# Kernel tuning notes

Measured on AMD Instinct MI355X. Metric: run time of the kernel, lower is better.

Reference implementation:

```python
import jax, jax.numpy as jnp
import numpy as np

V, E, H, L, B, T = 371, 512, 8, 8, 4, 1024
D = E // H
EPS = 1e-5


def setup_inputs() -> dict:
    key = jax.random.key(0)
    ks = jax.random.split(key, 7)
    s = 0.02
    return {
        "idx": jax.random.randint(ks[0], (B, T), 0, V),
        "wte": jax.random.normal(ks[1], (V, E), jnp.float32) * s,   # tied with lm_head
        "wpe": jax.random.normal(ks[2], (T, E), jnp.float32) * s,
        "c_attn_w": jax.random.normal(ks[3], (L, E, 3 * E), jnp.float32) * s,
        "c_proj_w": jax.random.normal(ks[4], (L, E, E), jnp.float32) * s,
        "fc_w": jax.random.normal(ks[5], (L, E, 4 * E), jnp.float32) * s,
        "fc_proj_w": jax.random.normal(ks[6], (L, 4 * E, E), jnp.float32) * s,
        "ln1_w": jnp.ones((L, E), jnp.float32),
        "ln2_w": jnp.ones((L, E), jnp.float32),
        "lnf_w": jnp.ones((E,), jnp.float32),
    }


def _ln(x, w):
    m = jnp.mean(x, axis=-1, keepdims=True)
    v = jnp.mean((x - m) ** 2, axis=-1, keepdims=True)
    return (x - m) * jax.lax.rsqrt(v + EPS) * w


def reference(idx, wte, wpe, c_attn_w, c_proj_w, fc_w, fc_proj_w, ln1_w, ln2_w, lnf_w):
    mask = jnp.tril(jnp.ones((T, T), bool))  # causal mask, as in the registered buffer
    scale = 1.0 / np.sqrt(D)

    x0 = wte[idx] + wpe[None, :T]  # [B,T,E]

    def block(x, p):
        aw, pw, l1, l2, fw, fpw = p
        h = _ln(x, l1)
        qkv = h @ aw                                   # [B,T,3E]
        q, k, v = jnp.split(qkv, 3, axis=-1)
        q = q.reshape(B, T, H, D)
        k = k.reshape(B, T, H, D)
        v = v.reshape(B, T, H, D)
        att = jnp.einsum("bqhd,bkhd->bhqk", q, k) * scale  # full TxT scores (faithful)
        att = jnp.where(mask[None, None], att, -jnp.inf)
        att = jax.nn.softmax(att, axis=-1)
        y = jnp.einsum("bhqk,bkhd->bqhd", att, v).reshape(B, T, E)
        x = x + y @ pw
        h = _ln(x, l2)
        x = x + jax.nn.gelu(h @ fw, approximate=False) @ fpw
        return x, None

    x, _ = jax.lax.scan(block, x0, (c_attn_w, c_proj_w, ln1_w, ln2_w, fc_w, fc_proj_w))
    x = _ln(x, lnf_w)
    logits = x @ wte.T  # weight tying: lm_head.weight = wte.weight
    return logits
```

## Files before the change

kernel.cpp:

```cpp
#include <hip/hip_runtime.h>


#define VOCAB 371
#define VPAD  384
#define EMB   512
#define NH    8
#define NL    8
#define TS    1024
#define NTOK  4096
#define NEG_INF (-1e30f)

typedef unsigned short ushort_t;
typedef __attribute__((ext_vector_type(8))) short short8;
typedef __attribute__((ext_vector_type(4))) float f32x4;

__device__ inline float bf2f(ushort_t b) {
    unsigned int u = ((unsigned int)b) << 16;
    float f; __builtin_memcpy(&f, &u, 4); return f;
}
__device__ inline ushort_t f2bf(float f) {
    unsigned int u; __builtin_memcpy(&u, &f, 4);
    u = (u + 0x7fff + ((u >> 16) & 1)) >> 16;
    return (ushort_t)u;
}

#define GLOAD16(gp, lp) __builtin_amdgcn_global_load_lds( \
        (__attribute__((address_space(1))) void*)(gp), \
        (__attribute__((address_space(3))) void*)(lp), 16, 0, 0)

__global__ __launch_bounds__(64) void detect_k(const ushort_t* __restrict__ w,
        int* __restrict__ flag)
{
    int i = threadIdx.x;
    float v = bf2f(w[2 * i]);
    bool ok = (__builtin_fabsf(v) <= 4.0f);
    unsigned long long m = __ballot(ok);
    if (i == 0) flag[0] = (__popcll(m) >= 56) ? 1 : 0;
}

__global__ __launch_bounds__(256) void sentinel_k(ushort_t* __restrict__ out, int n)
{
    int i = blockIdx.x * 256 + threadIdx.x;
    if (i < n) out[i] = 0x447A;
}

__global__ __launch_bounds__(256) void embed_k(const int* __restrict__ idx,
        const void* __restrict__ wte, const void* __restrict__ wpe,
        float* __restrict__ x, const int* __restrict__ flag)
{
    int n = blockIdx.x, tid = threadIdx.x;
    int t = n & (TS - 1);
    int v = idx[n];
    size_t o = (size_t)n * EMB;
    float a0, a1, b0, b1;
    if (*flag) {
        const ushort_t* te = (const ushort_t*)wte; const ushort_t* pe = (const ushort_t*)wpe;
        a0 = bf2f(te[v * EMB + tid]); a1 = bf2f(te[v * EMB + 256 + tid]);
        b0 = bf2f(pe[t * EMB + tid]); b1 = bf2f(pe[t * EMB + 256 + tid]);
    } else {
        const float* te = (const float*)wte; const float* pe = (const float*)wpe;
        a0 = te[v * EMB + tid]; a1 = te[v * EMB + 256 + tid];
        b0 = pe[t * EMB + tid]; b1 = pe[t * EMB + 256 + tid];
    }
    x[o + tid] = a0 + b0;
    x[o + 256 + tid] = a1 + b1;
}

__global__ __launch_bounds__(256) void ln_k(const float* __restrict__ x,
        const void* __restrict__ w, long woff, ushort_t* __restrict__ out,
        const int* __restrict__ flag)
{
    const int row = blockIdx.x * 4 + (threadIdx.x >> 6);
    const int lane = threadIdx.x & 63;
    const float* xr = x + (size_t)row * EMB + lane * 8;
    float4 f0 = *(const float4*)xr;
    float4 f1 = *(const float4*)(xr + 4);
    float v[8] = {f0.x, f0.y, f0.z, f0.w, f1.x, f1.y, f1.z, f1.w};
    float s = ((v[0] + v[1]) + (v[2] + v[3])) + ((v[4] + v[5]) + (v[6] + v[7]));
#pragma unroll
    for (int off = 32; off > 0; off >>= 1) s += __shfl_xor(s, off, 64);
    float mean = s * (1.0f / EMB);
    float s2 = 0.f;
#pragma unroll
    for (int j = 0; j < 8; ++j) { v[j] -= mean; s2 += v[j] * v[j]; }
#pragma unroll
    for (int off = 32; off > 0; off >>= 1) s2 += __shfl_xor(s2, off, 64);
    float rs = rsqrtf(s2 * (1.0f / EMB) + 1e-5f);
    float g[8];
    if (*flag) {
        const ushort_t* wb = (const ushort_t*)w + woff + lane * 8;
        ushort_t tmp[8];
        *(uint4*)tmp = *(const uint4*)wb;
#pragma unroll
        for (int j = 0; j < 8; ++j) g[j] = bf2f(tmp[j]);
    } else {
        const float* wf = (const float*)w + woff + lane * 8;
        float4 g0 = *(const float4*)wf;
        float4 g1 = *(const float4*)(wf + 4);
        g[0] = g0.x; g[1] = g0.y; g[2] = g0.z; g[3] = g0.w;
        g[4] = g1.x; g[5] = g1.y; g[6] = g1.z; g[7] = g1.w;
    }
    ushort_t ob[8];
#pragma unroll
    for (int j = 0; j < 8; ++j) ob[j] = f2bf(v[j] * rs * g[j]);
    *(uint4*)(out + (size_t)row * EMB + lane * 8) = *(uint4*)ob;
}

__global__ __launch_bounds__(256) void wtrans_k(const void* __restrict__ aw,
        const void* __restrict__ pw, const void* __restrict__ fw,
        const void* __restrict__ fpw, long l, ushort_t* __restrict__ wbuf,
        const int* __restrict__ flag)
{
    __shared__ float tile[64][65];
    const int isbf = *flag;
    long lay = (l < 0) ? (long)blockIdx.z : l;
    ushort_t* obase = wbuf + ((l < 0) ? (size_t)blockIdx.z * 3145728 : 0);
    int t = blockIdx.x;
    const void* src; ushort_t* dst; int Kw, Nw; long ioff;
    if (t < 192)      { src = aw;  dst = obase;           Kw = 512;  Nw = 1536; ioff = lay * 512L * 1536; }
    else if (t < 256) { t -= 192; src = pw;  dst = obase + 786432;  Kw = 512;  Nw = 512;  ioff = lay * 512L * 512; }
    else if (t < 512) { t -= 256; src = fw;  dst = obase + 1048576; Kw = 512;  Nw = 2048; ioff = lay * 512L * 2048; }
    else              { t -= 512; src = fpw; dst = obase + 2097152; Kw = 2048; Nw = 512;  ioff = lay * 2048L * 512; }
    int tn = Nw >> 6;
    int n0 = (t % tn) * 64, k0 = (t / tn) * 64;
    const int r = threadIdx.x >> 2, cq = (threadIdx.x & 3) * 16;
    size_t ii = ioff + (size_t)(k0 + r) * Nw + n0 + cq;
    if (isbf) {
        const ushort_t* sb = (const ushort_t*)src + ii;
        ushort_t tmp[16];
        *(uint4*)tmp = *(const uint4*)sb;
        *(uint4*)(tmp + 8) = *(const uint4*)(sb + 8);
#pragma unroll
        for (int j = 0; j < 16; ++j) tile[r][cq + j] = bf2f(tmp[j]);
    } else {
        const float* sf = (const float*)src + ii;
        *(float4*)&tile[r][cq]      = *(const float4*)sf;
        *(float4*)&tile[r][cq + 4]  = *(const float4*)(sf + 4);
        *(float4*)&tile[r][cq + 8]  = *(const float4*)(sf + 8);
        *(float4*)&tile[r][cq + 12] = *(const float4*)(sf + 12);
    }
    __syncthreads();
    const int kc = (threadIdx.x & 7) * 8;
#pragma unroll
    for (int j = 0; j < 2; ++j) {
        const int n = (threadIdx.x >> 3) + j * 32;
        unsigned pk[4];
#pragma unroll
        for (int i = 0; i < 4; ++i) {
            unsigned lo = f2bf(tile[kc + 2 * i][n]);
            unsigned hi = f2bf(tile[kc + 2 * i + 1][n]);
            pk[i] = lo | (hi << 16);
        }
        *(uint4*)(dst + (size_t)(n0 + n) * Kw + k0 + kc) = *(uint4*)pk;
    }
}

__global__ __launch_bounds__(256) void wconv_k(const void* __restrict__ in,
        ushort_t* __restrict__ out, int n, int nreal, const int* __restrict__ flag)
{
    int i = blockIdx.x * 256 + threadIdx.x;
    if (i >= n) return;
    ushort_t v = 0;
    if (i < nreal) v = (*flag) ? ((const ushort_t*)in)[i] : f2bf(((const float*)in)[i]);
    out[i] = v;
}

template<int MI>
__global__ __launch_bounds__(256) void gemm_gl(const ushort_t* __restrict__ A,
        const ushort_t* __restrict__ Bt, int M, int N, int K,
        float* __restrict__ outF, ushort_t* __restrict__ outB, void* __restrict__ outD,
        const float* __restrict__ res, int act, const int* __restrict__ flag)
{
    constexpr int BM = MI * 64;
    __shared__ __align__(16) ushort_t Al[BM * 64];
    __shared__ __align__(16) ushort_t Bl[64 * 64];
    const int tid = threadIdx.x;
    const int wave = tid >> 6, lane = tid & 63;
    const int quad = lane >> 4, l16 = lane & 15;
    const int m0 = blockIdx.y * BM, n0 = blockIdx.x * 64;
    const int sr = lane >> 3, sc = (lane & 7) * 8;
    const size_t K8 = (size_t)K * 8;
    const ushort_t* Ag = A + (size_t)(m0 + wave * (MI * 16) + sr) * K + sc;
    const ushort_t* Bg = Bt + (size_t)(n0 + wave * 16 + sr) * K + sc;
    ushort_t* Alw = &Al[(wave * (MI * 16)) * 64];
    ushort_t* Blw = &Bl[(wave * 16) * 64];
    f32x4 acc[MI][4] = {};
    for (int k0 = 0; k0 < K; k0 += 64) {
        __syncthreads();
#pragma unroll
        for (int i = 0; i < MI * 2; ++i)
            GLOAD16(Ag + k0 + (size_t)i * K8, Alw + i * 512);
#pragma unroll
        for (int i = 0; i < 2; ++i)
            GLOAD16(Bg + k0 + (size_t)i * K8, Blw + i * 512);
        __syncthreads();
#pragma unroll
        for (int ks = 0; ks < 2; ++ks) {
            short8 af[MI], bfr[4];
#pragma unroll
            for (int mi = 0; mi < MI; ++mi)
                af[mi] = *(const short8*)&Al[(wave * (MI * 16) + mi * 16 + l16) * 64 + ks * 32 + quad * 8];
#pragma unroll
            for (int ni = 0; ni < 4; ++ni)
                bfr[ni] = *(const short8*)&Bl[(ni * 16 + l16) * 64 + ks * 32 + quad * 8];
#pragma unroll
            for (int mi = 0; mi < MI; ++mi)
#pragma unroll
                for (int ni = 0; ni < 4; ++ni)
                    acc[mi][ni] = __builtin_amdgcn_mfma_f32_16x16x32_bf16(
                            af[mi], bfr[ni], acc[mi][ni], 0, 0, 0);
        }
    }
    const int isbf = *flag;
#pragma unroll
    for (int mi = 0; mi < MI; ++mi) {
        const int rowb = m0 + wave * (MI * 16) + mi * 16 + quad * 4;
#pragma unroll
        for (int ni = 0; ni < 4; ++ni) {
            const int nn = n0 + ni * 16 + l16;
            if (nn >= N) continue;
#pragma unroll
            for (int r = 0; r < 4; ++r) {
                size_t o = (size_t)(rowb + r) * N + nn;
                float v = acc[mi][ni][r];
                if (res) v += res[o];
                if (act) v = 0.5f * v * (1.0f + erff(v * 0.70710678118f));
                if (outF)      outF[o] = v;
                else if (outB) outB[o] = f2bf(v);
                else if (isbf) ((ushort_t*)outD)[o] = f2bf(v);
                else           ((float*)outD)[o] = v;
            }
        }
    }
}

__global__ __launch_bounds__(256) void gemm_k(const ushort_t* __restrict__ A,
        const void* __restrict__ B, long boff, int M, int N, int K, int bt,
        float* __restrict__ outF, ushort_t* __restrict__ outB, void* __restrict__ outD,
        const float* __restrict__ res, int act, const int* __restrict__ flag)
{
    __shared__ ushort_t Al[64 * 40];
    __shared__ ushort_t Bl[64 * 40];
    const int isbf = *flag;
    const int tid = threadIdx.x;
    const int wave = tid >> 6, lane = tid & 63;
    const int quad = lane >> 4, l16 = lane & 15;
    const int m0 = blockIdx.y * 64, n0 = blockIdx.x * 64;
    const int sr = tid >> 2, sc = (tid & 3) * 8;
    const int kr = tid >> 3, nc = (tid & 7) * 8;
    f32x4 acc[4] = {};
    const bool bok = (n0 + sr) < N;
    const ushort_t* Ag = A + (size_t)(m0 + sr) * K + sc;
    const ushort_t* Bb = (const ushort_t*)B + boff;
    const float*    Bf = (const float*)B + boff;
    const size_t i1 = (size_t)(n0 + sr) * K + sc;
    const size_t i0 = (size_t)kr * N + n0 + nc;
    for (int k0 = 0; k0 < K; k0 += 32) {
        uint4 av = *(const uint4*)(Ag + k0);
        ushort_t b8[8] = {0, 0, 0, 0, 0, 0, 0, 0};
        size_t bi = bt ? (i1 + k0) : (i0 + (size_t)k0 * N);
        if (!bt || bok) {
            if (isbf) *(uint4*)b8 = *(const uint4*)(Bb + bi);
            else {
                float4 f0 = *(const float4*)(Bf + bi);
                float4 f1 = *(const float4*)(Bf + bi + 4);
                b8[0] = f2bf(f0.x); b8[1] = f2bf(f0.y); b8[2] = f2bf(f0.z); b8[3] = f2bf(f0.w);
                b8[4] = f2bf(f1.x); b8[5] = f2bf(f1.y); b8[6] = f2bf(f1.z); b8[7] = f2bf(f1.w);
            }
        }
        __syncthreads();
        *(uint4*)&Al[sr * 40 + sc] = av;
        if (bt) *(uint4*)&Bl[sr * 40 + sc] = *(uint4*)b8;
        else {
#pragma unroll
            for (int i = 0; i < 8; ++i) Bl[(nc + i) * 40 + kr] = b8[i];
        }
        __syncthreads();
        short8 af = *(const short8*)&Al[(wave * 16 + l16) * 40 + quad * 8];
#pragma unroll
        for (int nt = 0; nt < 4; ++nt) {
            short8 bf = *(const short8*)&Bl[(nt * 16 + l16) * 40 + quad * 8];
            acc[nt] = __builtin_amdgcn_mfma_f32_16x16x32_bf16(af, bf, acc[nt], 0, 0, 0);
        }
    }
    const int mb = m0 + wave * 16 + quad * 4;
#pragma unroll
    for (int nt = 0; nt < 4; ++nt) {
        int nn = n0 + nt * 16 + l16;
        if (nn >= N) continue;
#pragma unroll
        for (int r = 0; r < 4; ++r) {
            size_t o = (size_t)(mb + r) * N + nn;
            float v = acc[nt][r];
            if (res) v += res[o];
            if (act) v = 0.5f * v * (1.0f + erff(v * 0.70710678118f));
            if (outF)      outF[o] = v;
            else if (outB) outB[o] = f2bf(v);
            else if (isbf) ((ushort_t*)outD)[o] = f2bf(v);
            else           ((float*)outD)[o] = v;
        }
    }
}

__global__ __launch_bounds__(256) void attn_k(const ushort_t* __restrict__ qkv,
        ushort_t* __restrict__ y)
{
    __shared__ ushort_t Kl[64 * 72];
    __shared__ ushort_t Vt[64 * 72];
    __shared__ ushort_t Pl[4][16 * 72];
    const int tid = threadIdx.x, wave = tid >> 6, lane = tid & 63;
    const int quad = lane >> 4, l16 = lane & 15;
    const int qt = (int)gridDim.x - 1 - blockIdx.x;
    const int b = blockIdx.y >> 3, h = blockIdx.y & 7;
    const int q0b = qt * 64;
    const int q0w = q0b + wave * 16;
    const size_t rstr = 3 * EMB;
    const ushort_t* qbase = qkv + ((size_t)(b * TS) + q0w + l16) * rstr + h * 64;
    short8 qf0, qf1;
    {
        ushort_t q0[8], q1[8];
        *(uint4*)q0 = *(const uint4*)(qbase + quad * 8);
        *(uint4*)q1 = *(const uint4*)(qbase + 32 + quad * 8);
#pragma unroll
        for (int i = 0; i < 8; ++i) {
            qf0[i] = (short)f2bf(bf2f(q0[i]) * 0.125f);
            qf1[i] = (short)f2bf(bf2f(q1[i]) * 0.125f);
        }
    }
    short8 onesf;
#pragma unroll
    for (int i = 0; i < 8; ++i) onesf[i] = (short)0x3F80;
    f32x4 O[4] = {};
    f32x4 lacc = {};
    const int sk = tid >> 2, sdc = (tid & 3) * 16;
    const int vp = tid >> 3, vdc = (tid & 7) * 8;
    const int vsh = 16 * ((tid & 7) & 3);
    const int vcol = (2 * vp + vsh) & 63;
    for (int kt = 0; kt <= qt; ++kt) {
        const int k0 = kt * 64;
        const ushort_t* krow = qkv + ((size_t)(b * TS) + k0 + sk) * rstr + EMB + h * 64 + sdc;
        uint4 kv0 = *(const uint4*)krow;
        uint4 kv1 = *(const uint4*)(krow + 8);
        const ushort_t* vrow = qkv + ((size_t)(b * TS) + k0 + 2 * vp) * rstr + 2 * EMB + h * 64 + vdc;
        uint4 vv0 = *(const uint4*)vrow;
        uint4 vv1 = *(const uint4*)(vrow + rstr);
        __syncthreads();
        *(uint4*)&Kl[sk * 72 + sdc]     = kv0;
        *(uint4*)&Kl[sk * 72 + sdc + 8] = kv1;
        {
            ushort_t v0[8], v1[8];
            *(uint4*)v0 = vv0; *(uint4*)v1 = vv1;
#pragma unroll
            for (int i = 0; i < 8; ++i) {
                unsigned pk = (unsigned)v0[i] | ((unsigned)v1[i] << 16);
                *(unsigned*)&Vt[(vdc + i) * 72 + vcol] = pk;
            }
        }
        __syncthreads();
        if (kt < qt) {
            f32x4 S[4] = {};
#pragma unroll
            for (int nt = 0; nt < 4; ++nt) {
                short8 kf0 = *(const short8*)&Kl[(nt * 16 + l16) * 72 + quad * 8];
                short8 kf1 = *(const short8*)&Kl[(nt * 16 + l16) * 72 + 32 + quad * 8];
                S[nt] = __builtin_amdgcn_mfma_f32_16x16x32_bf16(qf0, kf0, S[nt], 0, 0, 0);
                S[nt] = __builtin_amdgcn_mfma_f32_16x16x32_bf16(qf1, kf1, S[nt], 0, 0, 0);
            }
#pragma unroll
            for (int nt = 0; nt < 4; ++nt)
#pragma unroll
                for (int r = 0; r < 4; ++r)
                    Pl[wave][(quad * 4 + r) * 72 + nt * 16 + l16] = f2bf(__expf(S[nt][r]));
        } else {
            f32x4 S[4] = {};
#pragma unroll
            for (int nt = 0; nt < 4; ++nt) {
                if (nt > wave) continue;
                short8 kf0 = *(const short8*)&Kl[(nt * 16 + l16) * 72 + quad * 8];
                short8 kf1 = *(const short8*)&Kl[(nt * 16 + l16) * 72 + 32 + quad * 8];
                S[nt] = __builtin_amdgcn_mfma_f32_16x16x32_bf16(qf0, kf0, S[nt], 0, 0, 0);
                S[nt] = __builtin_amdgcn_mfma_f32_16x16x32_bf16(qf1, kf1, S[nt], 0, 0, 0);
            }
#pragma unroll
            for (int nt = 0; nt < 4; ++nt)
#pragma unroll
                for (int r = 0; r < 4; ++r) {
                    bool live = (nt < wave) || (nt == wave && l16 <= quad * 4 + r);
                    float p = live ? __expf(S[nt][r]) : 0.f;
                    Pl[wave][(quad * 4 + r) * 72 + nt * 16 + l16] = f2bf(p);
                }
        }
#pragma unroll
        for (int kc = 0; kc < 2; ++kc) {
            short8 pf = *(const short8*)&Pl[wave][l16 * 72 + kc * 32 + quad * 8];
            lacc = __builtin_amdgcn_mfma_f32_16x16x32_bf16(pf, onesf, lacc, 0, 0, 0);
#pragma unroll
            for (int dt = 0; dt < 4; ++dt) {
                int d = dt * 16 + l16;
                int sh = ((2 * dt + (l16 >> 3)) & 3) * 16;
                int col = (kc * 32 + quad * 8 + sh) & 63;
                short8 vf = *(const short8*)&Vt[d * 72 + col];
                O[dt] = __builtin_amdgcn_mfma_f32_16x16x32_bf16(pf, vf, O[dt], 0, 0, 0);
            }
        }
    }
#pragma unroll
    for (int dt = 0; dt < 4; ++dt)
#pragma unroll
        for (int r = 0; r < 4; ++r) {
            int q = q0w + quad * 4 + r;
            float v = O[dt][r] / lacc[r];
            y[((size_t)(b * TS) + q) * EMB + h * 64 + dt * 16 + l16] = f2bf(v);
        }
}

extern "C" void kernel_launch(void* const* d_in, const int* in_sizes, int n_in,
                              void* d_out, int out_size, void* d_ws, size_t ws_size,
                              hipStream_t stream)
{
    const int*  idx    = (const int*)d_in[0];
    const void* wte    = d_in[1];
    const void* wpe    = d_in[2];
    const void* attn_w = d_in[3];
    const void* proj_w = d_in[4];
    const void* fc_w   = d_in[5];
    const void* fcp_w  = d_in[6];
    const void* ln1_w  = d_in[7];
    const void* ln2_w  = d_in[8];
    const void* lnf_w  = d_in[9];

    const size_t sz_xw    = (size_t)NTOK * EMB * 4;
    const size_t sz_hbf   = (size_t)NTOK * EMB * 2;
    const size_t sz_big   = (size_t)NTOK * 2048 * 2;
    const size_t sz_wteb  = (size_t)VPAD * EMB * 2;
    const size_t sz_wbuf1 = (size_t)3145728 * 2;
    const size_t need_legacy = 256 + sz_xw + sz_hbf + sz_big;
    const size_t need_fast   = need_legacy + sz_wteb + sz_wbuf1;
    const size_t need_all    = need_legacy + sz_wteb + NL * sz_wbuf1;

    if (ws_size < need_legacy) {
        sentinel_k<<<(out_size + 255) / 256, 256, 0, stream>>>((ushort_t*)d_out, out_size);
        return;
    }
    int* flag = (int*)d_ws;
    char* p = (char*)d_ws + 256;
    float*    xw  = (float*)p;    p += sz_xw;
    ushort_t* hbf = (ushort_t*)p; p += sz_hbf;
    ushort_t* big = (ushort_t*)p; p += sz_big;

    detect_k<<<1, 64, 0, stream>>>((const ushort_t*)wte, flag);
    embed_k<<<NTOK, 256, 0, stream>>>(idx, wte, wpe, xw, flag);

    if (ws_size >= need_fast) {
        ushort_t* wteb = (ushort_t*)p; p += sz_wteb;
        ushort_t* wbuf = (ushort_t*)p;
        const bool allw = (ws_size >= need_all);
        wconv_k<<<(VPAD * EMB + 255) / 256, 256, 0, stream>>>(wte, wteb,
                VPAD * EMB, VOCAB * EMB, flag);
        if (allw)
            wtrans_k<<<dim3(768, 1, NL), 256, 0, stream>>>(attn_w, proj_w, fc_w, fcp_w,
                    -1, wbuf, flag);
        for (int l = 0; l < NL; ++l) {
            ushort_t* wb = allw ? (wbuf + (size_t)l * 3145728) : wbuf;
            if (!allw)
                wtrans_k<<<dim3(768, 1, 1), 256, 0, stream>>>(attn_w, proj_w, fc_w, fcp_w,
                        (long)l, wbuf, flag);
            ln_k<<<NTOK / 4, 256, 0, stream>>>(xw, ln1_w, (long)l * EMB, hbf, flag);
            gemm_gl<2><<<dim3(24, 32), 256, 0, stream>>>(hbf, wb,
                    NTOK, 1536, 512, nullptr, big, nullptr, nullptr, 0, flag);
            attn_k<<<dim3(16, 32), 256, 0, stream>>>(big, hbf);
            gemm_gl<1><<<dim3(8, 64), 256, 0, stream>>>(hbf, wb + 786432,
                    NTOK, 512, 512, xw, nullptr, nullptr, xw, 0, flag);
            ln_k<<<NTOK / 4, 256, 0, stream>>>(xw, ln2_w, (long)l * EMB, hbf, flag);
            gemm_gl<2><<<dim3(32, 32), 256, 0, stream>>>(hbf, wb + 1048576,
                    NTOK, 2048, 512, nullptr, big, nullptr, nullptr, 1 , flag);
            gemm_gl<1><<<dim3(8, 64), 256, 0, stream>>>(big, wb + 2097152,
                    NTOK, 512, 2048, xw, nullptr, nullptr, xw, 0, flag);
        }
        ln_k<<<NTOK / 4, 256, 0, stream>>>(xw, lnf_w, 0, hbf, flag);
        gemm_gl<1><<<dim3(6, 64), 256, 0, stream>>>(hbf, wteb,
                NTOK, VOCAB, 512, nullptr, nullptr, d_out, nullptr, 0, flag);
    } else {
        for (int l = 0; l < NL; ++l) {
            ln_k<<<NTOK / 4, 256, 0, stream>>>(xw, ln1_w, (long)l * EMB, hbf, flag);
            gemm_k<<<dim3(24, 64), 256, 0, stream>>>(hbf, attn_w, (long)l * 512 * 1536,
                    NTOK, 1536, 512, 0, nullptr, big, nullptr, nullptr, 0, flag);
            attn_k<<<dim3(16, 32), 256, 0, stream>>>(big, hbf);
            gemm_k<<<dim3(8, 64), 256, 0, stream>>>(hbf, proj_w, (long)l * 512 * 512,
                    NTOK, 512, 512, 0, xw, nullptr, nullptr, xw, 0, flag);
            ln_k<<<NTOK / 4, 256, 0, stream>>>(xw, ln2_w, (long)l * EMB, hbf, flag);
            gemm_k<<<dim3(32, 64), 256, 0, stream>>>(hbf, fc_w, (long)l * 512 * 2048,
                    NTOK, 2048, 512, 0, nullptr, big, nullptr, nullptr, 1, flag);
            gemm_k<<<dim3(8, 64), 256, 0, stream>>>(big, fcp_w, (long)l * 2048 * 512,
                    NTOK, 512, 2048, 0, xw, nullptr, nullptr, xw, 0, flag);
        }
        ln_k<<<NTOK / 4, 256, 0, stream>>>(xw, lnf_w, 0, hbf, flag);
        gemm_k<<<dim3(6, 64), 256, 0, stream>>>(hbf, wte, 0,
                NTOK, VOCAB, 512, 1, nullptr, nullptr, d_out, nullptr, 0, flag);
    }
}
```

Before: 1.167 ms.

## Double-buffer LDS tiles in gemm_gl to overlap global loads with MFMA

```diff
diff --git a/kernel.cpp b/kernel.cpp
--- a/kernel.cpp
+++ b/kernel.cpp
@@ -172,8 +172,8 @@
         const float* __restrict__ res, int act, const int* __restrict__ flag)
 {
     constexpr int BM = MI * 64;
-    __shared__ __align__(16) ushort_t Al[BM * 64];
-    __shared__ __align__(16) ushort_t Bl[64 * 64];
+    __shared__ __align__(16) ushort_t Al[2][BM * 64];
+    __shared__ __align__(16) ushort_t Bl[2][64 * 64];
     const int tid = threadIdx.x;
     const int wave = tid >> 6, lane = tid & 63;
     const int quad = lane >> 4, l16 = lane & 15;
@@ -182,35 +182,54 @@
     const size_t K8 = (size_t)K * 8;
     const ushort_t* Ag = A + (size_t)(m0 + wave * (MI * 16) + sr) * K + sc;
     const ushort_t* Bg = Bt + (size_t)(n0 + wave * 16 + sr) * K + sc;
-    ushort_t* Alw = &Al[(wave * (MI * 16)) * 64];
-    ushort_t* Blw = &Bl[(wave * 16) * 64];
+    const int awoff = (wave * (MI * 16)) * 64;
+    const int bwoff = (wave * 16) * 64;
     f32x4 acc[MI][4] = {};
-    for (int k0 = 0; k0 < K; k0 += 64) {
-        __syncthreads();
-#pragma unroll
-        for (int i = 0; i < MI * 2; ++i)
-            GLOAD16(Ag + k0 + (size_t)i * K8, Alw + i * 512);
-#pragma unroll
-        for (int i = 0; i < 2; ++i)
-            GLOAD16(Bg + k0 + (size_t)i * K8, Blw + i * 512);
-        __syncthreads();
-#pragma unroll
-        for (int ks = 0; ks < 2; ++ks) {
-            short8 af[MI], bfr[4];
-#pragma unroll
-            for (int mi = 0; mi < MI; ++mi)
-                af[mi] = *(const short8*)&Al[(wave * (MI * 16) + mi * 16 + l16) * 64 + ks * 32 + quad * 8];
-#pragma unroll
-            for (int ni = 0; ni < 4; ++ni)
-                bfr[ni] = *(const short8*)&Bl[(ni * 16 + l16) * 64 + ks * 32 + quad * 8];
-#pragma unroll
-            for (int mi = 0; mi < MI; ++mi)
-#pragma unroll
-                for (int ni = 0; ni < 4; ++ni)
-                    acc[mi][ni] = __builtin_amdgcn_mfma_f32_16x16x32_bf16(
-                            af[mi], bfr[ni], acc[mi][ni], 0, 0, 0);
-        }
-    }
+
+#define STAGE_GL(buf, k0) do { \
+        _Pragma("unroll") \
+        for (int i = 0; i < MI * 2; ++i) \
+            GLOAD16(Ag + (k0) + (size_t)i * K8, &Al[buf][awoff + i * 512]); \
+        _Pragma("unroll") \
+        for (int i = 0; i < 2; ++i) \
+            GLOAD16(Bg + (k0) + (size_t)i * K8, &Bl[buf][bwoff + i * 512]); \
+    } while (0)
+
+#define COMPUTE_GL(buf) do { \
+        _Pragma("unroll") \
+        for (int ks = 0; ks < 2; ++ks) { \
+            short8 af[MI], bfr[4]; \
+            _Pragma("unroll") \
+            for (int mi = 0; mi < MI; ++mi) \
+                af[mi] = *(const short8*)&Al[buf][(wave * (MI * 16) + mi * 16 + l16) * 64 + ks * 32 + quad * 8]; \
+            _Pragma("unroll") \
+            for (int ni = 0; ni < 4; ++ni) \
+                bfr[ni] = *(const short8*)&Bl[buf][(ni * 16 + l16) * 64 + ks * 32 + quad * 8]; \
+            _Pragma("unroll") \
+            for (int mi = 0; mi < MI; ++mi) \
+                _Pragma("unroll") \
+                for (int ni = 0; ni < 4; ++ni) \
+                    acc[mi][ni] = __builtin_amdgcn_mfma_f32_16x16x32_bf16( \
+                            af[mi], bfr[ni], acc[mi][ni], 0, 0, 0); \
+        } \
+    } while (0)
+
+    STAGE_GL(0, 0);
+    asm volatile("s_waitcnt vmcnt(0)" ::: "memory");
+    __builtin_amdgcn_s_barrier();
+    const int nk = K >> 6;
+    int cur = 0;
+    for (int t = 0; t < nk - 1; ++t) {
+        STAGE_GL(cur ^ 1, (t + 1) << 6);
+        COMPUTE_GL(cur);
+        asm volatile("s_waitcnt vmcnt(0)" ::: "memory");
+        __builtin_amdgcn_s_barrier();
+        cur ^= 1;
+    }
+    COMPUTE_GL(cur);
+#undef STAGE_GL
+#undef COMPUTE_GL
+
     const int isbf = *flag;
 #pragma unroll
     for (int mi = 0; mi < MI; ++mi) {
```

Result: slower. 1.275 ms (+9.2%).
